# Optimization experiments

Measured on AMD Instinct MI355X. Metric: run time of the kernel, lower is better.

## Reference

```python
import jax, jax.numpy as jnp
import numpy as np

N, D, H = 8192, 1280, 16
K = D // H          # head_dim = 80
S = 16              # number of packed segments
L = N // S          # tokens per segment = 512
SCALE = K ** -0.5


def rotate_half(x):
    x1, x2 = jnp.split(x, 2, axis=-1)
    return jnp.concatenate([-x2, x1], axis=-1)


def setup_inputs() -> dict:
    key = jax.random.key(0)
    ks = jax.random.split(key, 4)
    # RoPE tables over head_dim, shared by all heads
    inv_freq = 1.0 / (10000.0 ** (jnp.arange(0, K, 2, dtype=jnp.float32) / K))
    freqs = jnp.outer(jnp.arange(N, dtype=jnp.float32), inv_freq)  # [N, K/2]
    emb = jnp.concatenate([freqs, freqs], axis=-1)                 # [N, K]
    return {
        "hidden_ND": jax.random.normal(ks[0], (N, D), jnp.float32),
        "cu_seqlens": jnp.arange(S + 1, dtype=jnp.int32) * L,      # equal-length segments
        "cos_NK": jnp.cos(emb),
        "sin_NK": jnp.sin(emb),
        "qkv_w": jax.random.normal(ks[1], (D, 3 * D), jnp.float32) * (D ** -0.5),
        "qkv_b": jnp.zeros((3 * D,), jnp.float32),
        "proj_w": jax.random.normal(ks[2], (D, D), jnp.float32) * (D ** -0.5),
        "proj_b": jnp.zeros((D,), jnp.float32),
    }


def reference(hidden_ND, cu_seqlens, cos_NK, sin_NK, qkv_w, qkv_b, proj_w, proj_b):
    n = hidden_ND.shape[0]
    qkv = (hidden_ND @ qkv_w + qkv_b).reshape(n, 3, H, K)
    q, k, v = qkv[:, 0], qkv[:, 1], qkv[:, 2]          # each [N, H, K]
    cos = cos_NK[:, None, :]
    sin = sin_NK[:, None, :]
    q = q * cos + rotate_half(q) * sin
    k = k * cos + rotate_half(k) * sin
    # Block-diagonal attention over equal-length segments defined by cu_seqlens.
    num_seqs = cu_seqlens.shape[0] - 1
    seg_len = n // num_seqs
    qs = q.reshape(num_seqs, seg_len, H, K)
    ks_ = k.reshape(num_seqs, seg_len, H, K)
    vs = v.reshape(num_seqs, seg_len, H, K)
    logits = jnp.einsum('slhk,smhk->shlm', qs, ks_) * SCALE   # [S, H, L, L]
    w = jax.nn.softmax(logits.astype(jnp.float32), axis=-1).astype(logits.dtype)
    out = jnp.einsum('shlm,smhk->slhk', w, vs).reshape(n, H * K)
    return out @ proj_w + proj_b
```

## Files before the change

### kernel.cpp

```cpp
#include <hip/hip_runtime.h>

#define LOG2E 1.44269504088896340736f
#define ATT_SCALE 0.11180339887498949f

typedef _Float16 half8 __attribute__((ext_vector_type(8)));
typedef _Float16 half4v __attribute__((ext_vector_type(4)));
typedef __fp16 fp16x2 __attribute__((ext_vector_type(2)));
typedef float f32x4 __attribute__((ext_vector_type(4)));

#define MFMA(a, b, c) __builtin_amdgcn_mfma_f32_16x16x32_f16((a), (b), (c), 0, 0, 0)

__device__ __forceinline__ void async16(const _Float16* g, _Float16* l) {
  __builtin_amdgcn_global_load_lds(
      (const __attribute__((address_space(1))) unsigned int*)g,
      (__attribute__((address_space(3))) unsigned int*)l,
      16, 0, 0);
}

__global__ __launch_bounds__(256) void cvt_k(const float* __restrict__ in,
                                             _Float16* __restrict__ out, int n4) {
  int i = blockIdx.x * 256 + threadIdx.x;
  if (i < n4) {
    f32x4 v = ((const f32x4*)in)[i];
    half4v hv;
    hv[0] = (_Float16)v[0]; hv[1] = (_Float16)v[1];
    hv[2] = (_Float16)v[2]; hv[3] = (_Float16)v[3];
    ((half4v*)out)[i] = hv;
  }
}

__global__ __launch_bounds__(256) void transpose_cvt_k(const float* __restrict__ in,
                                                       _Float16* __restrict__ out,
                                                       int R, int C) {
  __shared__ float tile[32][33];
  const int tx = threadIdx.x & 31, ty = threadIdx.x >> 5;
  const int c0 = blockIdx.x * 32, r0 = blockIdx.y * 32;
#pragma unroll
  for (int i = 0; i < 32; i += 8)
    tile[ty + i][tx] = in[(size_t)(r0 + ty + i) * C + c0 + tx];
  __syncthreads();
#pragma unroll
  for (int i = 0; i < 32; i += 8)
    out[(size_t)(c0 + ty + i) * R + r0 + tx] = (_Float16)tile[tx][ty + i];
}

__global__ __launch_bounds__(256, 2) void gemm256_k(const _Float16* __restrict__ A,
                                                    const _Float16* __restrict__ BT,
                                                    const float* __restrict__ bias,
                                                    _Float16* __restrict__ Qf,
                                                    _Float16* __restrict__ Kf,
                                                    _Float16* __restrict__ VTf) {
  __shared__ _Float16 sA[256 * 32];
  __shared__ _Float16 sB[128 * 32];
  const int tid = threadIdx.x;
  const int wave = tid >> 6, lane = tid & 63;
  const int quad = lane >> 4, l16 = lane & 15;
  const int m0 = blockIdx.x * 256;
  const int n0 = blockIdx.y * 128;
  const int mq = (wave & 1) * 128, nq = (wave >> 1) * 64;
  const int KD = 1280;

  const int srcg = (lane & 3) ^ ((lane >> 3) & 3);
  const int rg = (quad ^ ((l16 >> 1) & 3)) * 8;

  f32x4 acc[8][4] = {};

  for (int kt = 0; kt < KD; kt += 32) {
#pragma unroll
    for (int c = 0; c < 4; ++c) {
      const int j = wave * 4 + c;
      const int row = j * 16 + (lane >> 2);
      async16(A + (size_t)(m0 + row) * KD + kt + srcg * 8, &sA[j * 512]);
    }
#pragma unroll
    for (int c = 0; c < 2; ++c) {
      const int j = wave * 2 + c;
      const int row = j * 16 + (lane >> 2);
      async16(BT + (size_t)(n0 + row) * KD + kt + srcg * 8, &sB[j * 512]);
    }
    __syncthreads();
    half8 af[8], bf[4];
#pragma unroll
    for (int i = 0; i < 8; ++i)
      af[i] = *(const half8*)&sA[(mq + i * 16 + l16) * 32 + rg];
#pragma unroll
    for (int j = 0; j < 4; ++j)
      bf[j] = *(const half8*)&sB[(nq + j * 16 + l16) * 32 + rg];
#pragma unroll
    for (int i = 0; i < 8; ++i)
#pragma unroll
      for (int j2 = 0; j2 < 4; ++j2)
        acc[i][j2] = MFMA(af[i], bf[j2], acc[i][j2]);
    __syncthreads();
  }

#pragma unroll
  for (int i = 0; i < 8; ++i) {
#pragma unroll
    for (int j2 = 0; j2 < 4; ++j2) {
      const int col = n0 + nq + j2 * 16 + l16;
      const float bv = bias[col];
      const int rowb = m0 + mq + i * 16 + quad * 4;
      const int which = col / 1280;
      const int rem = col - which * 1280;
      const int h = rem / 80;
      const int kk = rem - h * 80;
#pragma unroll
      for (int r = 0; r < 4; ++r) {
        const float v = acc[i][j2][r] + bv;
        const int mrow = rowb + r;
        const int s = mrow >> 9, l = mrow & 511;
        const int shh = s * 16 + h;
        if (which == 0)
          Qf[((size_t)shh * 512 + l) * 96 + kk] = (_Float16)v;
        else if (which == 1)
          Kf[((size_t)shh * 512 + l) * 96 + kk] = (_Float16)v;
        else
          VTf[((size_t)shh * 80 + kk) * 512 + l] = (_Float16)v;
      }
    }
  }
}

__global__ __launch_bounds__(256) void gemm_k(const _Float16* __restrict__ A,
                                              const _Float16* __restrict__ BT,
                                              const float* __restrict__ bias,
                                              float* __restrict__ Out) {
  __shared__ _Float16 sA[128 * 32];
  __shared__ _Float16 sB[128 * 32];
  const int tid = threadIdx.x;
  const int wave = tid >> 6, lane = tid & 63;
  const int quad = lane >> 4, l16 = lane & 15;
  const int m0 = blockIdx.x * 128;
  const int n0 = blockIdx.y * 128;
  const int mw = (wave & 1) * 64, nw = (wave >> 1) * 64;
  const int KD = 1280;

  const int srcg = (lane & 3) ^ ((lane >> 3) & 3);
  const int rg = (quad ^ ((l16 >> 1) & 3)) * 8;

  f32x4 acc[4][4] = {};

  for (int kt = 0; kt < KD; kt += 32) {
#pragma unroll
    for (int c = 0; c < 2; ++c) {
      const int j = wave * 2 + c;
      const int row = j * 16 + (lane >> 2);
      async16(A + (size_t)(m0 + row) * KD + kt + srcg * 8, &sA[j * 512]);
      async16(BT + (size_t)(n0 + row) * KD + kt + srcg * 8, &sB[j * 512]);
    }
    __syncthreads();
    half8 af[4], bf[4];
#pragma unroll
    for (int i = 0; i < 4; ++i) {
      af[i] = *(const half8*)&sA[(mw + i * 16 + l16) * 32 + rg];
      bf[i] = *(const half8*)&sB[(nw + i * 16 + l16) * 32 + rg];
    }
#pragma unroll
    for (int i = 0; i < 4; ++i)
#pragma unroll
      for (int j2 = 0; j2 < 4; ++j2)
        acc[i][j2] = MFMA(af[i], bf[j2], acc[i][j2]);
    __syncthreads();
  }

#pragma unroll
  for (int i = 0; i < 4; ++i) {
#pragma unroll
    for (int j2 = 0; j2 < 4; ++j2) {
      const int col = n0 + nw + j2 * 16 + l16;
      const float bv = bias[col];
      const int rowb = m0 + mw + i * 16 + quad * 4;
#pragma unroll
      for (int r = 0; r < 4; ++r)
        Out[(size_t)(rowb + r) * 1280 + col] = acc[i][j2][r] + bv;
    }
  }
}

__global__ __launch_bounds__(256) void rope_k(_Float16* __restrict__ Qf,
                                              _Float16* __restrict__ Kf,
                                              const float* __restrict__ cosNK,
                                              const float* __restrict__ sinNK) {
  const int gid = blockIdx.x * 256 + threadIdx.x;
  const int j = gid & 63;
  const int row = gid >> 6;
  const int qk = row >> 17;
  const int r = row & 131071;
  _Float16* buf = qk ? Kf : Qf;
  const int l = r & 511;
  const int s = r >> 13;
  const int t = s * 512 + l;
  const size_t base = (size_t)r * 96;
  if (j < 40) {
    const float v1 = (float)buf[base + j];
    const float v2 = (float)buf[base + j + 40];
    const float c1 = cosNK[t * 80 + j], s1 = sinNK[t * 80 + j];
    const float c2 = cosNK[t * 80 + j + 40], s2 = sinNK[t * 80 + j + 40];
    buf[base + j] = (_Float16)(v1 * c1 - v2 * s1);
    buf[base + j + 40] = (_Float16)(v2 * c2 + v1 * s2);
  } else if (j < 56) {
    buf[base + 40 + j] = (_Float16)0.f;
  }
}

__global__ __launch_bounds__(256) void attn_k(const _Float16* __restrict__ Qf,
                                              const _Float16* __restrict__ Kf,
                                              const _Float16* __restrict__ VTf,
                                              _Float16* __restrict__ attnA) {
  __shared__ _Float16 sP[128 * 72];
  __shared__ _Float16 sK[64 * 104];
  __shared__ _Float16 sV[96 * 72];
  const int tid = threadIdx.x;
  const int wave = tid >> 6, lane = tid & 63;
  const int quad = lane >> 4, l16 = lane & 15;
  const int shh = blockIdx.x;
  const int qt = blockIdx.y;
  const int h = shh & 15;
  const int s = shh >> 4;

  const _Float16* Qb = Qf + ((size_t)shh * 512 + qt * 128) * 96;
  const _Float16* Kb0 = Kf + (size_t)shh * 512 * 96;
  const _Float16* Vb0 = VTf + (size_t)shh * 80 * 512;

  const _Float16 c1h = (_Float16)(ATT_SCALE * LOG2E);
  half8 qf[2][3];
#pragma unroll
  for (int rt = 0; rt < 2; ++rt)
#pragma unroll
    for (int ks = 0; ks < 3; ++ks) {
      half8 t = *(const half8*)(Qb + (size_t)(wave * 32 + rt * 16 + l16) * 96 +
                                ks * 32 + quad * 8);
#pragma unroll
      for (int e = 0; e < 8; ++e) t[e] *= c1h;
      qf[rt][ks] = t;
    }

  for (int idx = tid; idx < 16 * 72; idx += 256) sV[80 * 72 + idx] = (_Float16)1.f;

  f32x4 o[2][6] = {};

  for (int kc = 0; kc < 8; ++kc) {
    __syncthreads();
    const _Float16* Kb = Kb0 + (size_t)kc * 64 * 96;
#pragma unroll
    for (int c = 0; c < 4; ++c) {
      const int j = wave + 4 * c;
      if (j < 13) {
        const int off = j * 1024 + lane * 16;
        const int krow = off / 208;
        const int kcol = off - krow * 208;
        if (kcol < 192)
          async16(Kb + (size_t)krow * 96 + (kcol >> 1), &sK[j * 512]);
      }
    }
#pragma unroll
    for (int c = 0; c < 3; ++c) {
      const int j = wave + 4 * c;
      const int off = j * 1024 + lane * 16;
      const int vrow = off / 144;
      const int colb = off - vrow * 144;
      if (vrow < 80 && colb < 128)
        async16(Vb0 + (size_t)vrow * 512 + kc * 64 + (colb >> 1), &sV[j * 512]);
    }
    __syncthreads();

    f32x4 sacc[2][4] = {};
#pragma unroll
    for (int mt = 0; mt < 4; ++mt) {
#pragma unroll
      for (int ks = 0; ks < 3; ++ks) {
        half8 kb = *(const half8*)&sK[(mt * 16 + l16) * 104 + ks * 32 + quad * 8];
        sacc[0][mt] = MFMA(kb, qf[0][ks], sacc[0][mt]);
        sacc[1][mt] = MFMA(kb, qf[1][ks], sacc[1][mt]);
      }
    }

#pragma unroll
    for (int rt = 0; rt < 2; ++rt) {
#pragma unroll
      for (int mt = 0; mt < 4; ++mt) {
        union { fp16x2 h2[2]; half4v h4; } u;
        u.h2[0] = __builtin_amdgcn_cvt_pkrtz(
            __builtin_amdgcn_exp2f(sacc[rt][mt][0]),
            __builtin_amdgcn_exp2f(sacc[rt][mt][1]));
        u.h2[1] = __builtin_amdgcn_cvt_pkrtz(
            __builtin_amdgcn_exp2f(sacc[rt][mt][2]),
            __builtin_amdgcn_exp2f(sacc[rt][mt][3]));
        *(half4v*)&sP[(wave * 32 + rt * 16 + l16) * 72 + mt * 16 + quad * 4] = u.h4;
      }
    }

#pragma unroll
    for (int ks = 0; ks < 2; ++ks) {
      half8 pa[2];
      pa[0] = *(const half8*)&sP[(wave * 32 + 0 + l16) * 72 + ks * 32 + quad * 8];
      pa[1] = *(const half8*)&sP[(wave * 32 + 16 + l16) * 72 + ks * 32 + quad * 8];
#pragma unroll
      for (int ft = 0; ft < 6; ++ft) {
        half8 vb = *(const half8*)&sV[(ft * 16 + l16) * 72 + ks * 32 + quad * 8];
        o[0][ft] = MFMA(pa[0], vb, o[0][ft]);
        o[1][ft] = MFMA(pa[1], vb, o[1][ft]);
      }
    }
  }

#pragma unroll
  for (int rt = 0; rt < 2; ++rt) {
#pragma unroll
    for (int r = 0; r < 4; ++r) {
      const float inv = 1.0f / o[rt][5][r];
      const int token = s * 512 + qt * 128 + wave * 32 + rt * 16 + quad * 4 + r;
#pragma unroll
      for (int ft = 0; ft < 5; ++ft)
        attnA[(size_t)token * 1280 + h * 80 + ft * 16 + l16] =
            (_Float16)(o[rt][ft][r] * inv);
    }
  }
}

extern "C" void kernel_launch(void* const* d_in, const int* in_sizes, int n_in,
                              void* d_out, int out_size, void* d_ws, size_t ws_size,
                              hipStream_t stream) {
  (void)in_sizes; (void)n_in; (void)out_size; (void)ws_size;
  const float* hidden = (const float*)d_in[0];
  const float* cosNK = (const float*)d_in[2];
  const float* sinNK = (const float*)d_in[3];
  const float* qkv_w = (const float*)d_in[4];
  const float* qkv_b = (const float*)d_in[5];
  const float* proj_w = (const float*)d_in[6];
  const float* proj_b = (const float*)d_in[7];
  float* out = (float*)d_out;

  char* ws = (char*)d_ws;
  _Float16* hA    = (_Float16*)(ws);
  _Float16* wT    = (_Float16*)(ws + 20971520);
  _Float16* projT = (_Float16*)(ws + 30801920);
  _Float16* Qf    = (_Float16*)(ws + 34078720);
  _Float16* Kf    = (_Float16*)(ws + 59244544);
  _Float16* VTf   = (_Float16*)(ws + 84410368);
  _Float16* attnA = (_Float16*)(ws + 105381888);

  cvt_k<<<10240, 256, 0, stream>>>(hidden, hA, 2621440);
  transpose_cvt_k<<<dim3(120, 40), 256, 0, stream>>>(qkv_w, wT, 1280, 3840);
  transpose_cvt_k<<<dim3(40, 40), 256, 0, stream>>>(proj_w, projT, 1280, 1280);
  gemm256_k<<<dim3(32, 30), 256, 0, stream>>>(hA, wT, qkv_b, Qf, Kf, VTf);
  rope_k<<<65536, 256, 0, stream>>>(Qf, Kf, cosNK, sinNK);
  attn_k<<<dim3(256, 4), 256, 0, stream>>>(Qf, Kf, VTf, attnA);
  gemm_k<<<dim3(64, 10), 256, 0, stream>>>(attnA, projT, proj_b, out);
}
```

Before: 366.4 us.

## Rewrite QKV GEMM as double-buffered 256x256 tile with phased MFMA scheduling

The QKV projection GEMM moves from 256x128 tiles with 4 waves and a single LDS buffer to 256x256 tiles with 8 waves, K-steps of 64, and double-buffered LDS with XOR swizzling. Each iteration is split into four phases that interleave async global-to-LDS loads for the next tiles with MFMA sub-blocks. Manual waitcnt, barriers and setprio control the overlap, and a block-index swizzle improves L2 locality. The aim is to hide global-load latency behind compute and raise arithmetic intensity. In exchange, hand-counted vmcnt values and heavy register and LDS use (128KB LDS) risk hazards and lower occupancy.

```diff
diff --git a/kernel.cpp b/kernel.cpp
--- a/kernel.cpp
+++ b/kernel.cpp
@@ -16,6 +16,22 @@
       (__attribute__((address_space(3))) unsigned int*)l,
       16, 0, 0);
 }
+
+#define FENCE() asm volatile("" ::: "memory")
+#define PH_MID()                                         \
+  do {                                                   \
+    FENCE();                                             \
+    __builtin_amdgcn_s_barrier();                        \
+    asm volatile("s_waitcnt lgkmcnt(0)" ::: "memory");   \
+    __builtin_amdgcn_sched_barrier(0);                   \
+  } while (0)
+#define PH_END()                                         \
+  do {                                                   \
+    __builtin_amdgcn_sched_barrier(0);                   \
+    FENCE();                                             \
+    __builtin_amdgcn_s_barrier();                        \
+    FENCE();                                             \
+  } while (0)
 
 __global__ __launch_bounds__(256) void cvt_k(const float* __restrict__ in,
                                              _Float16* __restrict__ out, int n4) {
@@ -44,70 +60,144 @@
     out[(size_t)(c0 + ty + i) * R + r0 + tx] = (_Float16)tile[tx][ty + i];
 }
 
-__global__ __launch_bounds__(256, 2) void gemm256_k(const _Float16* __restrict__ A,
+__global__ __launch_bounds__(512, 2) void gemm256_k(const _Float16* __restrict__ A,
                                                     const _Float16* __restrict__ BT,
                                                     const float* __restrict__ bias,
                                                     _Float16* __restrict__ Qf,
                                                     _Float16* __restrict__ Kf,
                                                     _Float16* __restrict__ VTf) {
-  __shared__ _Float16 sA[256 * 32];
-  __shared__ _Float16 sB[128 * 32];
+  __shared__ _Float16 sA[2][2][128 * 64];
+  __shared__ _Float16 sB[2][2][128 * 64];
   const int tid = threadIdx.x;
   const int wave = tid >> 6, lane = tid & 63;
   const int quad = lane >> 4, l16 = lane & 15;
-  const int m0 = blockIdx.x * 256;
-  const int n0 = blockIdx.y * 128;
-  const int mq = (wave & 1) * 128, nq = (wave >> 1) * 64;
-  const int KD = 1280;
-
-  const int srcg = (lane & 3) ^ ((lane >> 3) & 3);
-  const int rg = (quad ^ ((l16 >> 1) & 3)) * 8;
+  const int wm = wave >> 2, wn = wave & 3;
+  const int bh = wn >> 1, brb = (wn & 1) * 64;
+  const int KD = 1280, NT = 20;
+
+  const int id = blockIdx.x;
+  const int swz = (id & 7) * 60 + (id >> 3);
+  const int tm = swz & 31, tn = swz >> 5;
+  const int m0 = tm * 256, n0 = tn * 256;
 
   f32x4 acc[8][4] = {};
 
-  for (int kt = 0; kt < KD; kt += 32) {
-#pragma unroll
-    for (int c = 0; c < 4; ++c) {
-      const int j = wave * 4 + c;
-      const int row = j * 16 + (lane >> 2);
-      async16(A + (size_t)(m0 + row) * KD + kt + srcg * 8, &sA[j * 512]);
-    }
+  auto stageA = [&](int buf, int half, int kt) {
 #pragma unroll
     for (int c = 0; c < 2; ++c) {
-      const int j = wave * 2 + c;
-      const int row = j * 16 + (lane >> 2);
-      async16(BT + (size_t)(n0 + row) * KD + kt + srcg * 8, &sB[j * 512]);
-    }
-    __syncthreads();
-    half8 af[8], bf[4];
-#pragma unroll
-    for (int i = 0; i < 8; ++i)
-      af[i] = *(const half8*)&sA[(mq + i * 16 + l16) * 32 + rg];
-#pragma unroll
-    for (int j = 0; j < 4; ++j)
-      bf[j] = *(const half8*)&sB[(nq + j * 16 + l16) * 32 + rg];
-#pragma unroll
-    for (int i = 0; i < 8; ++i)
-#pragma unroll
-      for (int j2 = 0; j2 < 4; ++j2)
-        acc[i][j2] = MFMA(af[i], bf[j2], acc[i][j2]);
-    __syncthreads();
-  }
-
-#pragma unroll
-  for (int i = 0; i < 8; ++i) {
-#pragma unroll
-    for (int j2 = 0; j2 < 4; ++j2) {
-      const int col = n0 + nq + j2 * 16 + l16;
+      const int s = c * 512 + wave * 64 + lane;
+      const int row = s >> 3;
+      const int lg = (s & 7) ^ (row & 7);
+      async16(A + (size_t)(m0 + half * 128 + row) * KD + kt * 64 + lg * 8,
+              &sA[buf][half][(size_t)(c * 512 + wave * 64) * 8]);
+    }
+  };
+  auto stageB = [&](int buf, int half, int kt) {
+#pragma unroll
+    for (int c = 0; c < 2; ++c) {
+      const int s = c * 512 + wave * 64 + lane;
+      const int row = s >> 3;
+      const int lg = (s & 7) ^ (row & 7);
+      async16(BT + (size_t)(n0 + half * 128 + row) * KD + kt * 64 + lg * 8,
+              &sB[buf][half][(size_t)(c * 512 + wave * 64) * 8]);
+    }
+  };
+  auto ldA = [&](half8* af, const _Float16* hp, int rh) {
+#pragma unroll
+    for (int i = 0; i < 4; ++i)
+#pragma unroll
+      for (int kk = 0; kk < 2; ++kk) {
+        const int lrow = rh * 64 + i * 16 + l16;
+        const int pg = (kk * 4 + quad) ^ (l16 & 7);
+        af[i * 2 + kk] = *(const half8*)(hp + lrow * 64 + pg * 8);
+      }
+  };
+  auto ldB = [&](half8* bf, const _Float16* hp, int ch) {
+#pragma unroll
+    for (int j = 0; j < 2; ++j)
+#pragma unroll
+      for (int kk = 0; kk < 2; ++kk) {
+        const int brow = brb + ch * 32 + j * 16 + l16;
+        const int pg = (kk * 4 + quad) ^ (l16 & 7);
+        bf[j * 2 + kk] = *(const half8*)(hp + brow * 64 + pg * 8);
+      }
+  };
+  auto mmaq = [&](int r, int c, const half8* af, const half8* bf) {
+#pragma unroll
+    for (int i = 0; i < 4; ++i)
+#pragma unroll
+      for (int j = 0; j < 2; ++j)
+#pragma unroll
+        for (int kk = 0; kk < 2; ++kk)
+          acc[r * 4 + i][c * 2 + j] =
+              MFMA(af[i * 2 + kk], bf[j * 2 + kk], acc[r * 4 + i][c * 2 + j]);
+  };
+
+  stageA(0, 0, 0); stageA(0, 1, 0);
+  stageB(0, 0, 0); stageB(0, 1, 0);
+  stageB(1, 0, 1); stageB(1, 1, 1);
+  asm volatile("s_waitcnt vmcnt(4)" ::: "memory");
+  __builtin_amdgcn_s_barrier();
+  FENCE();
+
+  half8 af[8], bf0[4], bf1[4];
+#pragma unroll 2
+  for (int t = 0; t < NT; ++t) {
+    const int buf = t & 1;
+    const _Float16* aH = sA[buf][wm];
+    const _Float16* bH = sB[buf][bh];
+
+    ldA(af, aH, 0);
+    ldB(bf0, bH, 0);
+    if (t + 1 < NT) stageA(buf ^ 1, 0, t + 1);
+    PH_MID();
+    __builtin_amdgcn_s_setprio(1);
+    mmaq(0, 0, af, bf0);
+    __builtin_amdgcn_s_setprio(0);
+    PH_END();
+
+    ldB(bf1, bH, 1);
+    if (t + 1 < NT) stageA(buf ^ 1, 1, t + 1);
+    PH_MID();
+    __builtin_amdgcn_s_setprio(1);
+    mmaq(0, 1, af, bf1);
+    __builtin_amdgcn_s_setprio(0);
+    PH_END();
+
+    ldA(af, aH, 1);
+    if (t + 2 < NT) stageB(buf, 0, t + 2);
+    PH_MID();
+    __builtin_amdgcn_s_setprio(1);
+    mmaq(1, 1, af, bf1);
+    __builtin_amdgcn_s_setprio(0);
+    PH_END();
+
+    if (t + 2 < NT) stageB(buf, 1, t + 2);
+    if (t == NT - 2)
+      asm volatile("s_waitcnt vmcnt(0)" ::: "memory");
+    else if (t < NT - 2)
+      asm volatile("s_waitcnt vmcnt(4)" ::: "memory");
+    PH_MID();
+    __builtin_amdgcn_s_setprio(1);
+    mmaq(1, 0, af, bf0);
+    __builtin_amdgcn_s_setprio(0);
+    PH_END();
+  }
+
+#pragma unroll
+  for (int ridx = 0; ridx < 8; ++ridx) {
+#pragma unroll
+    for (int cidx = 0; cidx < 4; ++cidx) {
+      const int col = n0 + wn * 64 + cidx * 16 + l16;
       const float bv = bias[col];
-      const int rowb = m0 + mq + i * 16 + quad * 4;
+      const int rowb = m0 + wm * 128 + ridx * 16 + quad * 4;
       const int which = col / 1280;
       const int rem = col - which * 1280;
       const int h = rem / 80;
       const int kk = rem - h * 80;
 #pragma unroll
       for (int r = 0; r < 4; ++r) {
-        const float v = acc[i][j2][r] + bv;
+        const float v = acc[ridx][cidx][r] + bv;
         const int mrow = rowb + r;
         const int s = mrow >> 9, l = mrow & 511;
         const int shh = s * 16 + h;
@@ -344,7 +434,7 @@
   cvt_k<<<10240, 256, 0, stream>>>(hidden, hA, 2621440);
   transpose_cvt_k<<<dim3(120, 40), 256, 0, stream>>>(qkv_w, wT, 1280, 3840);
   transpose_cvt_k<<<dim3(40, 40), 256, 0, stream>>>(proj_w, projT, 1280, 1280);
-  gemm256_k<<<dim3(32, 30), 256, 0, stream>>>(hA, wT, qkv_b, Qf, Kf, VTf);
+  gemm256_k<<<480, 512, 0, stream>>>(hA, wT, qkv_b, Qf, Kf, VTf);
   rope_k<<<65536, 256, 0, stream>>>(Qf, Kf, cosNK, sinNK);
   attn_k<<<dim3(256, 4), 256, 0, stream>>>(Qf, Kf, VTf, attnA);
   gemm_k<<<dim3(64, 10), 256, 0, stream>>>(attnA, projT, proj_b, out);
```

Measured after the change: 373.3 us. Within noise of the previous version (+1.9%).

## Double-buffer QKV GEMM LDS with split-phase prefetch and XCD-aware tile mapping

Applied to the files above, without the earlier changes.

Rewrites the QKV projection GEMM main loop to double-buffer the A and B tiles in LDS. The next K-slice is prefetched asynchronously while MFMAs run on the current one, using two half-iterations split by barriers and explicit vmcnt waits. It also swaps the 2D grid for a 1D grid that maps blocks so that neighbouring M tiles land on the same XCD for L2 reuse, and raises wave priority around the MFMA bursts. Doubling the shared memory per block may reduce occupancy, and the hand-written waitcnt scheme is fragile.

```diff
diff --git a/kernel.cpp b/kernel.cpp
--- a/kernel.cpp
+++ b/kernel.cpp
@@ -16,6 +16,14 @@
       (__attribute__((address_space(3))) unsigned int*)l,
       16, 0, 0);
 }
+
+#define FENCE() asm volatile("" ::: "memory")
+#define PHB()                                   \
+  do {                                          \
+    FENCE();                                    \
+    __builtin_amdgcn_s_barrier();               \
+    FENCE();                                    \
+  } while (0)
 
 __global__ __launch_bounds__(256) void cvt_k(const float* __restrict__ in,
                                              _Float16* __restrict__ out, int n4) {
@@ -50,64 +58,113 @@
                                                     _Float16* __restrict__ Qf,
                                                     _Float16* __restrict__ Kf,
                                                     _Float16* __restrict__ VTf) {
-  __shared__ _Float16 sA[256 * 32];
-  __shared__ _Float16 sB[128 * 32];
+  __shared__ _Float16 sA[2][256 * 32];
+  __shared__ _Float16 sB[2][128 * 32];
   const int tid = threadIdx.x;
   const int wave = tid >> 6, lane = tid & 63;
   const int quad = lane >> 4, l16 = lane & 15;
-  const int m0 = blockIdx.x * 256;
-  const int n0 = blockIdx.y * 128;
-  const int mq = (wave & 1) * 128, nq = (wave >> 1) * 64;
-  const int KD = 1280;
-
-  const int srcg = (lane & 3) ^ ((lane >> 3) & 3);
-  const int rg = (quad ^ ((l16 >> 1) & 3)) * 8;
+  const int wm = wave >> 1, wn = wave & 1;
+  const int KD = 1280, NT = 40;
+
+  const int id = blockIdx.x;
+  const int xcd = id & 7;
+  const int qq = (id >> 3) & 3;
+  const int tn = id >> 5;
+  const int tm = xcd * 4 + qq;
+  const int m0 = tm * 256, n0 = tn * 128;
 
   f32x4 acc[8][4] = {};
 
-  for (int kt = 0; kt < KD; kt += 32) {
+  auto stageA = [&](int buf, int kt) {
 #pragma unroll
     for (int c = 0; c < 4; ++c) {
-      const int j = wave * 4 + c;
-      const int row = j * 16 + (lane >> 2);
-      async16(A + (size_t)(m0 + row) * KD + kt + srcg * 8, &sA[j * 512]);
-    }
+      const int s = c * 256 + tid;
+      const int row = s >> 2;
+      const int lg = (s & 3) ^ (row & 3);
+      async16(A + (size_t)(m0 + row) * KD + kt * 32 + lg * 8,
+              &sA[buf][(size_t)(c * 256 + wave * 64) * 8]);
+    }
+  };
+  auto stageB = [&](int buf, int kt) {
 #pragma unroll
     for (int c = 0; c < 2; ++c) {
-      const int j = wave * 2 + c;
-      const int row = j * 16 + (lane >> 2);
-      async16(BT + (size_t)(n0 + row) * KD + kt + srcg * 8, &sB[j * 512]);
-    }
-    __syncthreads();
-    half8 af[8], bf[4];
-#pragma unroll
-    for (int i = 0; i < 8; ++i)
-      af[i] = *(const half8*)&sA[(mq + i * 16 + l16) * 32 + rg];
-#pragma unroll
-    for (int j = 0; j < 4; ++j)
-      bf[j] = *(const half8*)&sB[(nq + j * 16 + l16) * 32 + rg];
-#pragma unroll
-    for (int i = 0; i < 8; ++i)
-#pragma unroll
-      for (int j2 = 0; j2 < 4; ++j2)
-        acc[i][j2] = MFMA(af[i], bf[j2], acc[i][j2]);
-    __syncthreads();
-  }
-
-#pragma unroll
-  for (int i = 0; i < 8; ++i) {
-#pragma unroll
-    for (int j2 = 0; j2 < 4; ++j2) {
-      const int col = n0 + nq + j2 * 16 + l16;
+      const int s = c * 256 + tid;
+      const int row = s >> 2;
+      const int lg = (s & 3) ^ (row & 3);
+      async16(BT + (size_t)(n0 + row) * KD + kt * 32 + lg * 8,
+              &sB[buf][(size_t)(c * 256 + wave * 64) * 8]);
+    }
+  };
+  auto ldA = [&](half8* af, const _Float16* base, int rh) {
+#pragma unroll
+    for (int i = 0; i < 4; ++i) {
+      const int row = wm * 128 + rh * 64 + i * 16 + l16;
+      const int pg = quad ^ (l16 & 3);
+      af[i] = *(const half8*)(base + row * 32 + pg * 8);
+    }
+  };
+  auto ldB = [&](half8* bf, const _Float16* base) {
+#pragma unroll
+    for (int j = 0; j < 4; ++j) {
+      const int row = wn * 64 + j * 16 + l16;
+      const int pg = quad ^ (l16 & 3);
+      bf[j] = *(const half8*)(base + row * 32 + pg * 8);
+    }
+  };
+  auto mmaq = [&](int rh, const half8* af, const half8* bf) {
+#pragma unroll
+    for (int i = 0; i < 4; ++i)
+#pragma unroll
+      for (int j = 0; j < 4; ++j)
+        acc[rh * 4 + i][j] = MFMA(af[i], bf[j], acc[rh * 4 + i][j]);
+  };
+
+  stageA(0, 0);
+  stageB(0, 0);
+  stageB(1, 1);
+  asm volatile("s_waitcnt vmcnt(2)" ::: "memory");
+
+  half8 af[4], bf[4];
+#pragma unroll 2
+  for (int t = 0; t < NT; ++t) {
+    const int buf = t & 1;
+    const _Float16* aB = &sA[buf][0];
+    const _Float16* bB = &sB[buf][0];
+
+    PHB();
+    ldA(af, aB, 0);
+    ldB(bf, bB);
+    if (t + 1 < NT) stageA(buf ^ 1, t + 1);
+    __builtin_amdgcn_s_setprio(1);
+    mmaq(0, af, bf);
+    __builtin_amdgcn_s_setprio(0);
+
+    PHB();
+    ldA(af, aB, 1);
+    if (t + 2 < NT) stageB(buf, t + 2);
+    if (t == NT - 2)
+      asm volatile("s_waitcnt vmcnt(0)" ::: "memory");
+    else if (t < NT - 2)
+      asm volatile("s_waitcnt vmcnt(2)" ::: "memory");
+    __builtin_amdgcn_s_setprio(1);
+    mmaq(1, af, bf);
+    __builtin_amdgcn_s_setprio(0);
+  }
+
+#pragma unroll
+  for (int ridx = 0; ridx < 8; ++ridx) {
+#pragma unroll
+    for (int cidx = 0; cidx < 4; ++cidx) {
+      const int col = n0 + wn * 64 + cidx * 16 + l16;
       const float bv = bias[col];
-      const int rowb = m0 + mq + i * 16 + quad * 4;
+      const int rowb = m0 + wm * 128 + ridx * 16 + quad * 4;
       const int which = col / 1280;
       const int rem = col - which * 1280;
       const int h = rem / 80;
       const int kk = rem - h * 80;
 #pragma unroll
       for (int r = 0; r < 4; ++r) {
-        const float v = acc[i][j2][r] + bv;
+        const float v = acc[ridx][cidx][r] + bv;
         const int mrow = rowb + r;
         const int s = mrow >> 9, l = mrow & 511;
         const int shh = s * 16 + h;
@@ -344,7 +401,7 @@
   cvt_k<<<10240, 256, 0, stream>>>(hidden, hA, 2621440);
   transpose_cvt_k<<<dim3(120, 40), 256, 0, stream>>>(qkv_w, wT, 1280, 3840);
   transpose_cvt_k<<<dim3(40, 40), 256, 0, stream>>>(proj_w, projT, 1280, 1280);
-  gemm256_k<<<dim3(32, 30), 256, 0, stream>>>(hA, wT, qkv_b, Qf, Kf, VTf);
+  gemm256_k<<<960, 256, 0, stream>>>(hA, wT, qkv_b, Qf, Kf, VTf);
   rope_k<<<65536, 256, 0, stream>>>(Qf, Kf, cosNK, sinNK);
   attn_k<<<dim3(256, 4), 256, 0, stream>>>(Qf, Kf, VTf, attnA);
   gemm_k<<<dim3(64, 10), 256, 0, stream>>>(attnA, projT, proj_b, out);
```

Result: no change. 363.0 us (-0.9%).
